# Performance work log

Hardware: AMD Instinct MI355X
Metric: run time of the kernel (lower is better)

Reference implementation:

```python
import jax, jax.numpy as jnp
import numpy as np

B = 64          # graphs per batch
N = 131072      # total nodes (B * 2048)
E = 524288      # total edges
V = 32000       # embedding vocab
D_IN = 256      # embed.output_size
D = 128         # GCN hidden size


def setup_inputs() -> dict:
    key = jax.random.key(0)
    ks = jax.random.split(key, 9)
    return {
        "node_tokens": jax.random.randint(ks[0], (N,), 0, V),
        "edge_index": jax.random.randint(ks[1], (2, E), 0, N),
        "embed_table": jax.random.normal(ks[2], (V, D_IN), jnp.float32),
        "W_node_w": jax.random.normal(ks[3], (D, D_IN), jnp.float32) * 0.02,
        "W_node_b": jax.random.normal(ks[4], (D,), jnp.float32) * 0.02,
        "conv1_w": jax.random.normal(ks[5], (D, D), jnp.float32) * 0.02,
        "conv1_b": jax.random.normal(ks[6], (D,), jnp.float32) * 0.02,
        "conv2_w": jax.random.normal(ks[7], (D, D), jnp.float32) * 0.02,
        "conv2_b": jax.random.normal(ks[8], (D,), jnp.float32) * 0.02,
    }


def _gcn_conv(x, src, dst, norm, W, b):
    # PyG GCNConv: linear first, then normalized scatter-add aggregation, then bias.
    x = x @ W.T                                        # [N, D]
    msg = x[src] * norm[:, None]                       # gather + per-edge scale
    out = jax.ops.segment_sum(msg, dst, num_segments=N)  # scatter-add at dst
    return out + b


def reference(node_tokens, edge_index, embed_table, W_node_w, W_node_b,
              conv1_w, conv1_b, conv2_w, conv2_b):
    # compute_node_features: embed lookup -> W_node linear (no mask path)
    x = embed_table[node_tokens] @ W_node_w.T + W_node_b   # [N, D]

    # GCNConv normalization with self-loops (shared by both layers)
    loop = jnp.arange(N)
    src = jnp.concatenate([edge_index[0], loop])
    dst = jnp.concatenate([edge_index[1], loop])
    deg = jax.ops.segment_sum(jnp.ones(E + N, x.dtype), dst, num_segments=N)
    dinv = jnp.where(deg > 0, jax.lax.rsqrt(deg), 0.0)
    norm = dinv[src] * dinv[dst]                           # [E+N]

    x = jax.nn.relu(_gcn_conv(x, src, dst, norm, conv1_w, conv1_b))
    x = _gcn_conv(x, src, dst, norm, conv2_w, conv2_b)

    # Unpad into [B, max_n, D]; equal-length graphs, no edge tokens -> reshape.
    n = N // B
    output = x.reshape(B, n, D)          # dropout_p=0 -> identity
    labels = node_tokens.reshape(B, n)
    labels_mask = jnp.ones((B, n), dtype=bool)
    label_node_ids = jnp.broadcast_to(jnp.arange(n), (B, n))
    return output, labels, labels_mask, label_node_ids
```

## Files before the change

### kernel.cpp

```cpp
#include <hip/hip_runtime.h>
#include <hip/hip_bf16.h>

#define N_NODES 131072
#define N_EDGES 524288
#define DHID    128
#define DIN     256

typedef __attribute__((ext_vector_type(8))) short short8;
typedef __attribute__((ext_vector_type(4))) float floatx4;

__device__ inline short bf16_rne(float f) {
    union { float f; unsigned u; } v; v.f = f;
    unsigned r = v.u + 0x7FFF + ((v.u >> 16) & 1);
    return (short)(r >> 16);
}
__device__ inline float bf16_to_f(short s) {
    union { unsigned u; float f; } v; v.u = ((unsigned)(unsigned short)s) << 16;
    return v.f;
}


__global__ __launch_bounds__(256) void count_edges(const int* __restrict__ dst,
                                                   int* __restrict__ counts) {
    int e = blockIdx.x * 256 + threadIdx.x;
    atomicAdd(&counts[dst[e]], 1);
}

__global__ __launch_bounds__(256) void scan1(const int* __restrict__ counts,
                                             int* __restrict__ offsets,
                                             int* __restrict__ bsums) {
    __shared__ int s[256];
    int i = blockIdx.x * 256 + threadIdx.x;
    int v = counts[i];
    s[threadIdx.x] = v;
    __syncthreads();
    for (int d = 1; d < 256; d <<= 1) {
        int t = (threadIdx.x >= d) ? s[threadIdx.x - d] : 0;
        __syncthreads();
        s[threadIdx.x] += t;
        __syncthreads();
    }
    offsets[i] = s[threadIdx.x] - v;
    if (threadIdx.x == 255) bsums[blockIdx.x] = s[255];
}

__global__ __launch_bounds__(512) void scan2(int* __restrict__ bsums) {
    __shared__ int s[512];
    int v = bsums[threadIdx.x];
    s[threadIdx.x] = v;
    __syncthreads();
    for (int d = 1; d < 512; d <<= 1) {
        int t = (threadIdx.x >= d) ? s[threadIdx.x - d] : 0;
        __syncthreads();
        s[threadIdx.x] += t;
        __syncthreads();
    }
    bsums[threadIdx.x] = s[threadIdx.x] - v;
}

__global__ __launch_bounds__(256) void scan3(const int* __restrict__ counts,
                                             int* __restrict__ offsets,
                                             int* __restrict__ cursor,
                                             float* __restrict__ dinv,
                                             const int* __restrict__ bsums) {
    int i = blockIdx.x * 256 + threadIdx.x;
    int off = offsets[i] + bsums[blockIdx.x];
    offsets[i] = off;
    cursor[i]  = off;
    dinv[i] = rsqrtf((float)(counts[i] + 1));
}

__global__ __launch_bounds__(256) void fill_csr(const int* __restrict__ src,
                                                const int* __restrict__ dst,
                                                int* __restrict__ cursor,
                                                int* __restrict__ csr_src) {
    int e = blockIdx.x * 256 + threadIdx.x;
    int d = dst[e];
    int p = atomicAdd(&cursor[d], 1);
    csr_src[p] = src[e];
}


__global__ __launch_bounds__(256) void convert_weights(const float* __restrict__ Wn,
                                                       const float* __restrict__ W1,
                                                       const float* __restrict__ W2,
                                                       short* __restrict__ Wnb,
                                                       short* __restrict__ W1b,
                                                       short* __restrict__ W2b) {
    int i = blockIdx.x * 256 + threadIdx.x;
    if (i < 32768)      Wnb[i] = bf16_rne(Wn[i]);
    else if (i < 49152) W1b[i - 32768] = bf16_rne(W1[i - 32768]);
    else                W2b[i - 49152] = bf16_rne(W2[i - 49152]);
}

__global__ __launch_bounds__(256) void convert_emb(const float* __restrict__ in,
                                                   short* __restrict__ outb) {
    size_t i = (size_t)(blockIdx.x * 256 + threadIdx.x) * 8;
    float4 v0 = *(const float4*)&in[i];
    float4 v1 = *(const float4*)&in[i + 4];
    short8 o;
    o[0] = bf16_rne(v0.x); o[1] = bf16_rne(v0.y);
    o[2] = bf16_rne(v0.z); o[3] = bf16_rne(v0.w);
    o[4] = bf16_rne(v1.x); o[5] = bf16_rne(v1.y);
    o[6] = bf16_rne(v1.z); o[7] = bf16_rne(v1.w);
    *(short8*)&outb[i] = o;
}


__global__ __launch_bounds__(256) void gemm_embed(const short* __restrict__ Ab,
                                                  const int* __restrict__ tok,
                                                  const short* __restrict__ Wb,
                                                  const float* __restrict__ bias,
                                                  short* __restrict__ out) {
    const int t = threadIdx.x;
    const int wid  = t >> 6;
    const int lane = t & 63;
    const int col  = lane & 15;
    const int quad = lane >> 4;
    const int base = blockIdx.x * 128 + wid * 32;

    const size_t row0 = (size_t)tok[base + col];
    const size_t row1 = (size_t)tok[base + 16 + col];

    floatx4 acc[2][8] = {};

#pragma unroll
    for (int kc = 0; kc < DIN / 32; ++kc) {
        const int ko = kc * 32 + quad * 8;
        short8 a0 = *(const short8*)&Ab[row0 * DIN + ko];
        short8 a1 = *(const short8*)&Ab[row1 * DIN + ko];
#pragma unroll
        for (int ft = 0; ft < 8; ++ft) {
            short8 b = *(const short8*)&Wb[(size_t)(ft * 16 + col) * DIN + ko];
            acc[0][ft] = __builtin_amdgcn_mfma_f32_16x16x32_bf16(a0, b, acc[0][ft], 0, 0, 0);
            acc[1][ft] = __builtin_amdgcn_mfma_f32_16x16x32_bf16(a1, b, acc[1][ft], 0, 0, 0);
        }
    }

#pragma unroll
    for (int ft = 0; ft < 8; ++ft) {
        float bv = bias[ft * 16 + col];
#pragma unroll
        for (int mt = 0; mt < 2; ++mt) {
            int mbase = base + mt * 16 + quad * 4;
#pragma unroll
            for (int r = 0; r < 4; ++r) {
                float v = acc[mt][ft][r] + bv;
                out[(size_t)(mbase + r) * DHID + ft * 16 + col] = bf16_rne(v);
            }
        }
    }
}


template <bool RELU, bool OUT_BF16>
__global__ __launch_bounds__(256) void fused_conv(const short* __restrict__ x,
                                                  const int* __restrict__ csr_src,
                                                  const int* __restrict__ offsets,
                                                  const int* __restrict__ counts,
                                                  const float* __restrict__ dinv,
                                                  const short* __restrict__ Wb,
                                                  const float* __restrict__ bias,
                                                  void* __restrict__ outp) {
    const int t = threadIdx.x;
    const int wid  = t >> 6;
    const int lane = t & 63;
    const int col  = lane & 15;
    const int quad = lane >> 4;
    const int base = (blockIdx.x * 4 + wid) * 16;
    const int node = base + col;

    const float di = dinv[node];
    const float s2 = di * di;
    const int beg = offsets[node];
    const int cnt = counts[node];

    float af[4][8];
    {
        const size_t xrow = (size_t)node * DHID + quad * 8;
#pragma unroll
        for (int c = 0; c < 4; ++c) {
            short8 v = *(const short8*)&x[xrow + c * 32];
#pragma unroll
            for (int j = 0; j < 8; ++j) af[c][j] = s2 * bf16_to_f(v[j]);
        }
    }

    int s_next = (cnt > 0) ? csr_src[beg] : 0;
    for (int e = 0; e < cnt; ++e) {
        int s = s_next;
        s_next = (e + 1 < cnt) ? csr_src[beg + e + 1] : 0;
        float w = di * dinv[s];
        const size_t srow = (size_t)s * DHID + quad * 8;
        short8 v0 = *(const short8*)&x[srow];
        short8 v1 = *(const short8*)&x[srow + 32];
        short8 v2 = *(const short8*)&x[srow + 64];
        short8 v3 = *(const short8*)&x[srow + 96];
#pragma unroll
        for (int j = 0; j < 8; ++j) {
            af[0][j] = fmaf(w, bf16_to_f(v0[j]), af[0][j]);
            af[1][j] = fmaf(w, bf16_to_f(v1[j]), af[1][j]);
            af[2][j] = fmaf(w, bf16_to_f(v2[j]), af[2][j]);
            af[3][j] = fmaf(w, bf16_to_f(v3[j]), af[3][j]);
        }
    }

    short8 a[4];
#pragma unroll
    for (int c = 0; c < 4; ++c)
#pragma unroll
        for (int j = 0; j < 8; ++j) a[c][j] = bf16_rne(af[c][j]);

    floatx4 acc[8] = {};
#pragma unroll
    for (int c = 0; c < 4; ++c) {
        const int ko = c * 32 + quad * 8;
#pragma unroll
        for (int ft = 0; ft < 8; ++ft) {
            short8 b = *(const short8*)&Wb[(size_t)(ft * 16 + col) * DHID + ko];
            acc[ft] = __builtin_amdgcn_mfma_f32_16x16x32_bf16(a[c], b, acc[ft], 0, 0, 0);
        }
    }

    short* outb = (short*)outp;
    float* outf = (float*)outp;
#pragma unroll
    for (int ft = 0; ft < 8; ++ft) {
        float bv = bias[ft * 16 + col];
#pragma unroll
        for (int r = 0; r < 4; ++r) {
            float v = acc[ft][r] + bv;
            if (RELU) v = fmaxf(v, 0.f);
            size_t idx = (size_t)(base + quad * 4 + r) * DHID + ft * 16 + col;
            if (OUT_BF16) outb[idx] = bf16_rne(v);
            else          outf[idx] = v;
        }
    }
}


__global__ __launch_bounds__(256) void meta_kernel(const int* __restrict__ tok,
                                                   float* __restrict__ out) {
    int i = blockIdx.x * 256 + threadIdx.x;
    const size_t L0 = (size_t)N_NODES * DHID;
    out[L0 + i]               = (float)tok[i];
    out[L0 + N_NODES + i]     = 1.0f;
    out[L0 + 2 * N_NODES + i] = (float)(i & 2047);
}


extern "C" void kernel_launch(void* const* d_in, const int* in_sizes, int n_in,
                              void* d_out, int out_size, void* d_ws, size_t ws_size,
                              hipStream_t stream) {
    const int*   tok  = (const int*)d_in[0];
    const int*   esrc = (const int*)d_in[1];
    const int*   edst = esrc + N_EDGES;
    const float* emb  = (const float*)d_in[2];
    const float* Wn   = (const float*)d_in[3];
    const float* bn   = (const float*)d_in[4];
    const float* W1   = (const float*)d_in[5];
    const float* b1   = (const float*)d_in[6];
    const float* W2   = (const float*)d_in[7];
    const float* b2   = (const float*)d_in[8];
    float* out = (float*)d_out;

    char* ws = (char*)d_ws;
    int*   counts  = (int*)(ws);
    int*   offsets = (int*)(ws + (1u << 19));
    int*   cursor  = (int*)(ws + (2u << 19));
    float* dinv    = (float*)(ws + (3u << 19));
    int*   bsums   = (int*)(ws + (4u << 19));
    int*   csr     = (int*)(ws + 3 * (1u << 20));
    short* Wnb     = (short*)(ws + 5 * (1u << 20));
    short* W1b     = (short*)(ws + 5 * (1u << 20) + (1u << 18));
    short* W2b     = (short*)(ws + 5 * (1u << 20) + (2u << 18));
    short* embb    = (short*)(ws + 6 * (1u << 20));
    short* x2b     = (short*)(ws + 24 * (1u << 20));
    short* xb      = (short*)d_out;

    hipMemsetAsync(counts, 0, N_NODES * sizeof(int), stream);
    count_edges<<<N_EDGES / 256, 256, 0, stream>>>(edst, counts);
    scan1<<<N_NODES / 256, 256, 0, stream>>>(counts, offsets, bsums);
    scan2<<<1, 512, 0, stream>>>(bsums);
    scan3<<<N_NODES / 256, 256, 0, stream>>>(counts, offsets, cursor, dinv, bsums);
    fill_csr<<<N_EDGES / 256, 256, 0, stream>>>(esrc, edst, cursor, csr);
    convert_weights<<<65536 / 256, 256, 0, stream>>>(Wn, W1, W2, Wnb, W1b, W2b);
    convert_emb<<<(32000 * 256 / 8) / 256, 256, 0, stream>>>(emb, embb);

    gemm_embed<<<N_NODES / 128, 256, 0, stream>>>(embb, tok, Wnb, bn, xb);
    fused_conv<true, true><<<N_NODES / 64, 256, 0, stream>>>(
        xb, csr, offsets, counts, dinv, W1b, b1, x2b);
    fused_conv<false, false><<<N_NODES / 64, 256, 0, stream>>>(
        x2b, csr, offsets, counts, dinv, W2b, b2, out);

    meta_kernel<<<N_NODES / 256, 256, 0, stream>>>(tok, out);
}
```

Measured before the change: 352.4 us.

## Pack dinv into CSR entries, unroll gather by two, vectorize output stores

The CSR now stores the source index together with that source's dinv, so the aggregation loop no longer does a dependent dinv gather per edge. The destination dinv is factored out and applied once at the end. The edge loop is unrolled by two so more row gathers are in flight at once. The weight-row mapping is permuted so each lane owns 8 contiguous output features, letting the embed GEMM and conv epilogues write vector stores instead of scattered scalar ones. In exchange the CSR doubles in size, the workspace is reshuffled, and register pressure rises.

```diff
diff --git a/kernel.cpp b/kernel.cpp
--- a/kernel.cpp
+++ b/kernel.cpp
@@ -73,11 +73,13 @@
 __global__ __launch_bounds__(256) void fill_csr(const int* __restrict__ src,
                                                 const int* __restrict__ dst,
                                                 int* __restrict__ cursor,
-                                                int* __restrict__ csr_src) {
+                                                const float* __restrict__ dinv,
+                                                int2* __restrict__ csr) {
     int e = blockIdx.x * 256 + threadIdx.x;
     int d = dst[e];
+    int s = src[e];
     int p = atomicAdd(&cursor[d], 1);
-    csr_src[p] = src[e];
+    csr[p] = make_int2(s, __float_as_int(dinv[s]));
 }
 
 
@@ -131,23 +133,26 @@
         short8 a1 = *(const short8*)&Ab[row1 * DIN + ko];
 #pragma unroll
         for (int ft = 0; ft < 8; ++ft) {
-            short8 b = *(const short8*)&Wb[(size_t)(ft * 16 + col) * DIN + ko];
+            short8 b = *(const short8*)&Wb[(size_t)(col * 8 + ft) * DIN + ko];
             acc[0][ft] = __builtin_amdgcn_mfma_f32_16x16x32_bf16(a0, b, acc[0][ft], 0, 0, 0);
             acc[1][ft] = __builtin_amdgcn_mfma_f32_16x16x32_bf16(a1, b, acc[1][ft], 0, 0, 0);
         }
     }
 
-#pragma unroll
-    for (int ft = 0; ft < 8; ++ft) {
-        float bv = bias[ft * 16 + col];
-#pragma unroll
-        for (int mt = 0; mt < 2; ++mt) {
-            int mbase = base + mt * 16 + quad * 4;
-#pragma unroll
-            for (int r = 0; r < 4; ++r) {
-                float v = acc[mt][ft][r] + bv;
-                out[(size_t)(mbase + r) * DHID + ft * 16 + col] = bf16_rne(v);
-            }
+    const float4 bv0 = *(const float4*)&bias[col * 8];
+    const float4 bv1 = *(const float4*)&bias[col * 8 + 4];
+    const float bb[8] = {bv0.x, bv0.y, bv0.z, bv0.w, bv1.x, bv1.y, bv1.z, bv1.w};
+
+#pragma unroll
+    for (int mt = 0; mt < 2; ++mt) {
+#pragma unroll
+        for (int r = 0; r < 4; ++r) {
+            const int row = base + mt * 16 + quad * 4 + r;
+            short8 o;
+#pragma unroll
+            for (int ft = 0; ft < 8; ++ft)
+                o[ft] = bf16_rne(acc[mt][ft][r] + bb[ft]);
+            *(short8*)&out[(size_t)row * DHID + col * 8] = o;
         }
     }
 }
@@ -155,7 +160,7 @@
 
 template <bool RELU, bool OUT_BF16>
 __global__ __launch_bounds__(256) void fused_conv(const short* __restrict__ x,
-                                                  const int* __restrict__ csr_src,
+                                                  const int2* __restrict__ csr,
                                                   const int* __restrict__ offsets,
                                                   const int* __restrict__ counts,
                                                   const float* __restrict__ dinv,
@@ -171,7 +176,6 @@
     const int node = base + col;
 
     const float di = dinv[node];
-    const float s2 = di * di;
     const int beg = offsets[node];
     const int cnt = counts[node];
 
@@ -182,26 +186,58 @@
         for (int c = 0; c < 4; ++c) {
             short8 v = *(const short8*)&x[xrow + c * 32];
 #pragma unroll
-            for (int j = 0; j < 8; ++j) af[c][j] = s2 * bf16_to_f(v[j]);
-        }
-    }
-
-    int s_next = (cnt > 0) ? csr_src[beg] : 0;
-    for (int e = 0; e < cnt; ++e) {
-        int s = s_next;
-        s_next = (e + 1 < cnt) ? csr_src[beg + e + 1] : 0;
-        float w = di * dinv[s];
-        const size_t srow = (size_t)s * DHID + quad * 8;
-        short8 v0 = *(const short8*)&x[srow];
-        short8 v1 = *(const short8*)&x[srow + 32];
-        short8 v2 = *(const short8*)&x[srow + 64];
-        short8 v3 = *(const short8*)&x[srow + 96];
+            for (int j = 0; j < 8; ++j) af[c][j] = di * bf16_to_f(v[j]);
+        }
+    }
+
+    int2 c0 = make_int2(0, 0), c1 = make_int2(0, 0);
+    if (cnt > 0) c0 = csr[beg];
+    if (cnt > 1) c1 = csr[beg + 1];
+    int e = 0;
+    for (; e + 2 <= cnt; e += 2) {
+        const int   s0 = c0.x, s1 = c1.x;
+        const float w0 = __int_as_float(c0.y);
+        const float w1 = __int_as_float(c1.y);
+        if (e + 2 < cnt) c0 = csr[beg + e + 2];
+        if (e + 3 < cnt) c1 = csr[beg + e + 3];
+        const size_t r0 = (size_t)s0 * DHID + quad * 8;
+        const size_t r1 = (size_t)s1 * DHID + quad * 8;
+        short8 u0 = *(const short8*)&x[r0];
+        short8 u1 = *(const short8*)&x[r0 + 32];
+        short8 u2 = *(const short8*)&x[r0 + 64];
+        short8 u3 = *(const short8*)&x[r0 + 96];
+        short8 v0 = *(const short8*)&x[r1];
+        short8 v1 = *(const short8*)&x[r1 + 32];
+        short8 v2 = *(const short8*)&x[r1 + 64];
+        short8 v3 = *(const short8*)&x[r1 + 96];
 #pragma unroll
         for (int j = 0; j < 8; ++j) {
-            af[0][j] = fmaf(w, bf16_to_f(v0[j]), af[0][j]);
-            af[1][j] = fmaf(w, bf16_to_f(v1[j]), af[1][j]);
-            af[2][j] = fmaf(w, bf16_to_f(v2[j]), af[2][j]);
-            af[3][j] = fmaf(w, bf16_to_f(v3[j]), af[3][j]);
+            af[0][j] = fmaf(w0, bf16_to_f(u0[j]), af[0][j]);
+            af[1][j] = fmaf(w0, bf16_to_f(u1[j]), af[1][j]);
+            af[2][j] = fmaf(w0, bf16_to_f(u2[j]), af[2][j]);
+            af[3][j] = fmaf(w0, bf16_to_f(u3[j]), af[3][j]);
+        }
+#pragma unroll
+        for (int j = 0; j < 8; ++j) {
+            af[0][j] = fmaf(w1, bf16_to_f(v0[j]), af[0][j]);
+            af[1][j] = fmaf(w1, bf16_to_f(v1[j]), af[1][j]);
+            af[2][j] = fmaf(w1, bf16_to_f(v2[j]), af[2][j]);
+            af[3][j] = fmaf(w1, bf16_to_f(v3[j]), af[3][j]);
+        }
+    }
+    if (e < cnt) {
+        const float w0 = __int_as_float(c0.y);
+        const size_t r0 = (size_t)c0.x * DHID + quad * 8;
+        short8 u0 = *(const short8*)&x[r0];
+        short8 u1 = *(const short8*)&x[r0 + 32];
+        short8 u2 = *(const short8*)&x[r0 + 64];
+        short8 u3 = *(const short8*)&x[r0 + 96];
+#pragma unroll
+        for (int j = 0; j < 8; ++j) {
+            af[0][j] = fmaf(w0, bf16_to_f(u0[j]), af[0][j]);
+            af[1][j] = fmaf(w0, bf16_to_f(u1[j]), af[1][j]);
+            af[2][j] = fmaf(w0, bf16_to_f(u2[j]), af[2][j]);
+            af[3][j] = fmaf(w0, bf16_to_f(u3[j]), af[3][j]);
         }
     }
 
@@ -209,7 +245,7 @@
 #pragma unroll
     for (int c = 0; c < 4; ++c)
 #pragma unroll
-        for (int j = 0; j < 8; ++j) a[c][j] = bf16_rne(af[c][j]);
+        for (int j = 0; j < 8; ++j) a[c][j] = bf16_rne(di * af[c][j]);
 
     floatx4 acc[8] = {};
 #pragma unroll
@@ -217,23 +253,42 @@
         const int ko = c * 32 + quad * 8;
 #pragma unroll
         for (int ft = 0; ft < 8; ++ft) {
-            short8 b = *(const short8*)&Wb[(size_t)(ft * 16 + col) * DHID + ko];
+            short8 b = *(const short8*)&Wb[(size_t)(col * 8 + ft) * DHID + ko];
             acc[ft] = __builtin_amdgcn_mfma_f32_16x16x32_bf16(a[c], b, acc[ft], 0, 0, 0);
         }
     }
 
+    const float4 bv0 = *(const float4*)&bias[col * 8];
+    const float4 bv1 = *(const float4*)&bias[col * 8 + 4];
+    const float bb[8] = {bv0.x, bv0.y, bv0.z, bv0.w, bv1.x, bv1.y, bv1.z, bv1.w};
     short* outb = (short*)outp;
     float* outf = (float*)outp;
 #pragma unroll
-    for (int ft = 0; ft < 8; ++ft) {
-        float bv = bias[ft * 16 + col];
-#pragma unroll
-        for (int r = 0; r < 4; ++r) {
-            float v = acc[ft][r] + bv;
-            if (RELU) v = fmaxf(v, 0.f);
-            size_t idx = (size_t)(base + quad * 4 + r) * DHID + ft * 16 + col;
-            if (OUT_BF16) outb[idx] = bf16_rne(v);
-            else          outf[idx] = v;
+    for (int r = 0; r < 4; ++r) {
+        const size_t row = (size_t)(base + quad * 4 + r) * DHID + col * 8;
+        if (OUT_BF16) {
+            short8 o;
+#pragma unroll
+            for (int ft = 0; ft < 8; ++ft) {
+                float v = acc[ft][r] + bb[ft];
+                if (RELU) v = fmaxf(v, 0.f);
+                o[ft] = bf16_rne(v);
+            }
+            *(short8*)&outb[row] = o;
+        } else {
+            float4 o0, o1;
+            o0.x = acc[0][r] + bb[0]; o0.y = acc[1][r] + bb[1];
+            o0.z = acc[2][r] + bb[2]; o0.w = acc[3][r] + bb[3];
+            o1.x = acc[4][r] + bb[4]; o1.y = acc[5][r] + bb[5];
+            o1.z = acc[6][r] + bb[6]; o1.w = acc[7][r] + bb[7];
+            if (RELU) {
+                o0.x = fmaxf(o0.x, 0.f); o0.y = fmaxf(o0.y, 0.f);
+                o0.z = fmaxf(o0.z, 0.f); o0.w = fmaxf(o0.w, 0.f);
+                o1.x = fmaxf(o1.x, 0.f); o1.y = fmaxf(o1.y, 0.f);
+                o1.z = fmaxf(o1.z, 0.f); o1.w = fmaxf(o1.w, 0.f);
+            }
+            *(float4*)&outf[row] = o0;
+            *(float4*)&outf[row + 4] = o1;
         }
     }
 }
@@ -270,11 +325,11 @@
     int*   cursor  = (int*)(ws + (2u << 19));
     float* dinv    = (float*)(ws + (3u << 19));
     int*   bsums   = (int*)(ws + (4u << 19));
-    int*   csr     = (int*)(ws + 3 * (1u << 20));
-    short* Wnb     = (short*)(ws + 5 * (1u << 20));
-    short* W1b     = (short*)(ws + 5 * (1u << 20) + (1u << 18));
-    short* W2b     = (short*)(ws + 5 * (1u << 20) + (2u << 18));
-    short* embb    = (short*)(ws + 6 * (1u << 20));
+    int2*  csr     = (int2*)(ws + 3 * (1u << 20));
+    short* Wnb     = (short*)(ws + 7 * (1u << 20));
+    short* W1b     = (short*)(ws + 7 * (1u << 20) + (1u << 16));
+    short* W2b     = (short*)(ws + 7 * (1u << 20) + 96 * 1024);
+    short* embb    = (short*)(ws + 7 * (1u << 20) + (1u << 18));
     short* x2b     = (short*)(ws + 24 * (1u << 20));
     short* xb      = (short*)d_out;
 
@@ -283,7 +338,7 @@
     scan1<<<N_NODES / 256, 256, 0, stream>>>(counts, offsets, bsums);
     scan2<<<1, 512, 0, stream>>>(bsums);
     scan3<<<N_NODES / 256, 256, 0, stream>>>(counts, offsets, cursor, dinv, bsums);
-    fill_csr<<<N_EDGES / 256, 256, 0, stream>>>(esrc, edst, cursor, csr);
+    fill_csr<<<N_EDGES / 256, 256, 0, stream>>>(esrc, edst, cursor, dinv, csr);
     convert_weights<<<65536 / 256, 256, 0, stream>>>(Wn, W1, W2, Wnb, W1b, W2b);
     convert_emb<<<(32000 * 256 / 8) / 256, 256, 0, stream>>>(emb, embb);
 
```

Result: no change. 349.4 us (-0.9%).
